# Optimization experiments

Measured on AMD Instinct MI355X. Metric: run time of the kernel, lower is better.

The kernel has to match this reference:

```python
import jax, jax.numpy as jnp
import numpy as np

E, N, D, H = 600000, 100000, 128, 128
LN_EPS = 1e-5


def setup_inputs() -> dict:
    key = jax.random.key(0)
    ks = jax.random.split(key, 10)
    inp = {
        "efeat": jax.random.normal(ks[0], (E, D), dtype=jnp.float32),
        "nfeat": jax.random.normal(ks[1], (N, D), dtype=jnp.float32),
        "src_idx": jax.random.randint(ks[2], (E,), 0, N, dtype=jnp.int64) if jax.config.jax_enable_x64 else jax.random.randint(ks[2], (E,), 0, N, dtype=jnp.int32),
        "dst_idx": jax.random.randint(ks[3], (E,), 0, N, dtype=jnp.int32),
        # MLP params: Linear(3D -> H) + SiLU, Linear(H -> D), LayerNorm(D)
        "W1": jax.random.normal(ks[4], (3 * D, H), dtype=jnp.float32) / np.sqrt(3 * D),
        "b1": jnp.zeros((H,), dtype=jnp.float32),
        "W2": jax.random.normal(ks[5], (H, D), dtype=jnp.float32) / np.sqrt(H),
        "b2": jnp.zeros((D,), dtype=jnp.float32),
        "ln_scale": jnp.ones((D,), dtype=jnp.float32),
        "ln_bias": jnp.zeros((D,), dtype=jnp.float32),
    }
    return inp


def _layernorm(x, scale, bias):
    mu = jnp.mean(x, axis=-1, keepdims=True)
    var = jnp.mean(jnp.square(x - mu), axis=-1, keepdims=True)
    return (x - mu) * jax.lax.rsqrt(var + LN_EPS) * scale + bias


def reference(efeat, nfeat, src_idx, dst_idx, W1, b1, W2, b2, ln_scale, ln_bias):
    # Gather per-edge source/destination node features (irregular access).
    src = nfeat[src_idx]              # [E, D]
    dst = nfeat[dst_idx]              # [E, D]
    # TMLP: equivalent to concat([efeat, src, dst]) @ W1; expressed as split GEMMs
    # so no [E, 3D] concat buffer is materialized.
    Wf, Ws, Wd = W1[:D], W1[D:2 * D], W1[2 * D:]
    h = efeat @ Wf + src @ Ws + dst @ Wd + b1   # [E, H]
    h = jax.nn.silu(h)
    y = h @ W2 + b2                              # [E, D]
    y = _layernorm(y, ln_scale, ln_bias)
    efeat_new = y + efeat                        # residual add
    return (efeat_new, nfeat)
```

## Files before the change

### kernel.cpp

```cpp
#include <hip/hip_runtime.h>
#include <stdint.h>

#define E_N 600000
#define N_N 100000

typedef short short8   __attribute__((ext_vector_type(8)));
typedef short short8a  __attribute__((ext_vector_type(8), may_alias));
typedef float floatx4  __attribute__((ext_vector_type(4)));
typedef float floatx2  __attribute__((ext_vector_type(2)));
typedef float floatx4a __attribute__((ext_vector_type(4), may_alias));
typedef float floatx8a __attribute__((ext_vector_type(8), may_alias));
typedef unsigned int uintx2  __attribute__((ext_vector_type(2)));
typedef unsigned int uintx2a __attribute__((ext_vector_type(2), may_alias));
typedef unsigned int uintx4  __attribute__((ext_vector_type(4)));
typedef unsigned int uintx4a __attribute__((ext_vector_type(4), may_alias));
typedef __bf16 bf16x4 __attribute__((ext_vector_type(4)));
typedef __bf16 bf16x8 __attribute__((ext_vector_type(8)));

static __device__ __forceinline__ unsigned short f2bf(float f){
  unsigned u = __builtin_bit_cast(unsigned, f);
  unsigned rnd = 0x7fffu + ((u >> 16) & 1u);
  return (unsigned short)((u + rnd) >> 16);
}
static __device__ __forceinline__ unsigned pk2(float a, float b){
  floatx2 f; f[0] = a; f[1] = b;
  typedef __bf16 bf16x2 __attribute__((ext_vector_type(2)));
  return __builtin_bit_cast(unsigned, __builtin_convertvector(f, bf16x2));
}

__global__ void prep_weights(const float* __restrict__ W1, const float* __restrict__ W2,
                             unsigned short* __restrict__ wall){
  int i = blockIdx.x * 256 + threadIdx.x;
  if (i < 384 * 128){
    int c = i / 384, k = i - c * 384;
    int win = k >> 6, kp = k & 63;
    wall[win * 8192 + (c * 32 + ((kp >> 1) ^ ((c & 7) << 2))) * 2 + (kp & 1)]
      = f2bf(W1[k * 128 + c]);
  } else {
    int j = i - 384 * 128;
    int c = j >> 7, k = j & 127;
    int win = 6 + (k >> 6), kp = k & 63;
    wall[win * 8192 + (c * 32 + ((kp >> 1) ^ ((c & 7) << 2))) * 2 + (kp & 1)]
      = f2bf(W2[k * 128 + c]);
  }
}

__global__ void prep_nfeat(const float* __restrict__ nf,
                           unsigned* __restrict__ nfbu,
                           float* __restrict__ out2){
  const int total = N_N * 128 / 4;
  int stride = gridDim.x * blockDim.x;
  for (int i = blockIdx.x * blockDim.x + threadIdx.x; i < total; i += stride){
    float4 v = reinterpret_cast<const float4*>(nf)[i];
    reinterpret_cast<float4*>(out2)[i] = v;
    nfbu[2 * i]     = pk2(v.x, v.y);
    nfbu[2 * i + 1] = pk2(v.z, v.w);
  }
}

static __device__ __forceinline__ void glds16(void* lds, const void* g){
  __builtin_amdgcn_global_load_lds((const __attribute__((address_space(1))) unsigned int*)g,
                                   (__attribute__((address_space(3))) unsigned int*)lds,
                                   16, 0, 0);
}

__global__ __launch_bounds__(256, 3) void fused_edge(
    const float* __restrict__ efeat,
    const int* __restrict__ src_idx, const int* __restrict__ dst_idx,
    const unsigned short* __restrict__ nfb,
    const unsigned short* __restrict__ wall,
    const float* __restrict__ b1, const float* __restrict__ b2,
    const float* __restrict__ lns, const float* __restrict__ lnb,
    float* __restrict__ out)
{
  __shared__ __align__(16) unsigned char smem[51200];
  unsigned int* wbuf  = (unsigned int*)smem;
  float*        cmisc = (float*)(smem + 49152);

  const int tid  = threadIdx.x;
  const int w    = tid >> 6;
  const int lane = tid & 63;
  const int r    = lane & 15;
  const int g    = lane >> 4;
  const int sw8  = (r & 7) << 2;

  unsigned int* tile = (unsigned int*)(smem + 32768 + w * 4096);

  auto stageW = [&](int b, int win){
    const unsigned char* src = (const unsigned char*)wall + win * 16384;
    #pragma unroll
    for (int rnd = 0; rnd < 4; ++rnd){
      int off = rnd * 4096 + tid * 16;
      glds16(smem + b * 16384 + off, src + off);
    }
  };

  stageW(0, 0);
  cmisc[tid]       = tid < 128 ? b1[tid]  : b2[tid - 128];
  cmisc[tid + 256] = tid < 128 ? lns[tid] : lnb[tid - 128];

  const int eb = blockIdx.x * 64 + w * 16;
  const int e0 = eb + r;
  int si = src_idx[e0];
  int di = dst_idx[e0];
  si = si < 0 ? 0 : (si >= N_N ? N_N - 1 : si);
  di = di < 0 ? 0 : (di >= N_N ? N_N - 1 : di);

  auto loadX_f32 = [&](const float* p) -> short8 {
    floatx8a f = *reinterpret_cast<const floatx8a*>(p);
    return __builtin_bit_cast(short8, __builtin_convertvector(f, bf16x8));
  };

  short8 xf[12];
  #pragma unroll
  for (int kf = 0; kf < 4; ++kf)
    xf[kf] = loadX_f32(efeat + (size_t)e0 * 128 + kf * 32 + 8 * g);
  #pragma unroll
  for (int kf = 0; kf < 4; ++kf)
    xf[4 + kf] = *reinterpret_cast<const short8a*>(nfb + (size_t)si * 128 + kf * 32 + 8 * g);
  #pragma unroll
  for (int kf = 0; kf < 4; ++kf)
    xf[8 + kf] = *reinterpret_cast<const short8a*>(nfb + (size_t)di * 128 + kf * 32 + 8 * g);

  __syncthreads();

  auto loadWL = [&](int b, int m, int k2) -> short8 {
    uintx4a v = *reinterpret_cast<const uintx4a*>(
        &wbuf[b * 4096 + (16 * m + r) * 32 + ((k2 * 16 + 4 * g) ^ sw8)]);
    return __builtin_bit_cast(short8, v);
  };

  floatx4 acc1[8];
  #pragma unroll
  for (int mi = 0; mi < 8; ++mi)
    acc1[mi] = (floatx4){0.f, 0.f, 0.f, 0.f};

  #pragma unroll
  for (int t = 0; t < 6; ++t){
    stageW((t + 1) & 1, t + 1);
    const int b = t & 1;
    #pragma unroll
    for (int k2 = 0; k2 < 2; ++k2){
      short8 x = xf[2 * t + k2];
      #pragma unroll
      for (int mi = 0; mi < 8; ++mi){
        short8 wf = loadWL(b, mi, k2);
        acc1[mi] = __builtin_amdgcn_mfma_f32_16x16x32_bf16(wf, x, acc1[mi], 0, 0, 0);
      }
    }
    if (t == 5){
      #pragma unroll
      for (int mi = 0; mi < 8; ++mi){
        floatx4 bb = *reinterpret_cast<const floatx4a*>(&cmisc[16 * mi + 4 * g]);
        floatx4 vv;
        #pragma unroll
        for (int q = 0; q < 4; ++q){
          float xx = acc1[mi][q] + bb[q];
          vv[q] = xx * __builtin_amdgcn_rcpf(1.f + __expf(-xx));
        }
        uintx2 pk = __builtin_bit_cast(uintx2, __builtin_convertvector(vv, bf16x4));
        *reinterpret_cast<uintx2a*>(&tile[r * 64 + ((8 * mi + 2 * g) ^ sw8)]) = pk;
      }
    }
    __syncthreads();
  }

  floatx4 acc2[8];
  #pragma unroll
  for (int mo = 0; mo < 8; ++mo)
    acc2[mo] = (floatx4){0.f, 0.f, 0.f, 0.f};

  #pragma unroll
  for (int t = 6; t < 8; ++t){
    if (t < 7) stageW((t + 1) & 1, t + 1);
    const int b = t & 1;
    #pragma unroll
    for (int k2 = 0; k2 < 2; ++k2){
      const int ks = 2 * (t - 6) + k2;
      uintx4a hv = *reinterpret_cast<const uintx4a*>(&tile[r * 64 + ((ks * 16 + 4 * g) ^ sw8)]);
      short8 hb = __builtin_bit_cast(short8, hv);
      #pragma unroll
      for (int mo = 0; mo < 8; ++mo){
        short8 wf = loadWL(b, mo, k2);
        acc2[mo] = __builtin_amdgcn_mfma_f32_16x16x32_bf16(wf, hb, acc2[mo], 0, 0, 0);
      }
    }
    if (t < 7) __syncthreads();
  }

  #pragma unroll
  for (int kf = 0; kf < 4; ++kf)
    *reinterpret_cast<uintx4a*>(&tile[r * 64 + ((16 * kf + 4 * g) ^ sw8)]) =
        __builtin_bit_cast(uintx4, xf[kf]);

  float s1 = 0.f, s2 = 0.f;
  #pragma unroll
  for (int mo = 0; mo < 8; ++mo){
    floatx4 bb = *reinterpret_cast<const floatx4a*>(&cmisc[128 + 16 * mo + 4 * g]);
    #pragma unroll
    for (int q = 0; q < 4; ++q){
      float v = acc2[mo][q] + bb[q];
      s1 += v; s2 += v * v;
    }
  }
  s1 += __shfl_xor(s1, 16); s2 += __shfl_xor(s2, 16);
  s1 += __shfl_xor(s1, 32); s2 += __shfl_xor(s2, 32);

  float mu   = s1 * (1.f / 128.f);
  float var  = s2 * (1.f / 128.f) - mu * mu;
  var = var > 0.f ? var : 0.f;
  float rstd = __builtin_amdgcn_rsqf(var + 1e-5f);

  float* op = out + (size_t)e0 * 128;
  #pragma unroll
  for (int mo = 0; mo < 8; ++mo){
    int c = 16 * mo + 4 * g;
    floatx4 bb = *reinterpret_cast<const floatx4a*>(&cmisc[128 + c]);
    floatx4 ls = *reinterpret_cast<const floatx4a*>(&cmisc[256 + c]);
    floatx4 lb = *reinterpret_cast<const floatx4a*>(&cmisc[384 + c]);
    uintx2a rv = *reinterpret_cast<const uintx2a*>(&tile[r * 64 + ((8 * mo + 2 * g) ^ sw8)]);
    floatx4 e4;
    e4[0] = __builtin_bit_cast(float, rv[0] << 16);
    e4[1] = __builtin_bit_cast(float, rv[0] & 0xffff0000u);
    e4[2] = __builtin_bit_cast(float, rv[1] << 16);
    e4[3] = __builtin_bit_cast(float, rv[1] & 0xffff0000u);
    floatx4 o4;
    #pragma unroll
    for (int q = 0; q < 4; ++q)
      o4[q] = (acc2[mo][q] + bb[q] - mu) * rstd * ls[q] + lb[q] + e4[q];
    *reinterpret_cast<floatx4a*>(op + c) = o4;
  }
}

extern "C" void kernel_launch(void* const* d_in, const int* in_sizes, int n_in,
                              void* d_out, int out_size, void* d_ws, size_t ws_size,
                              hipStream_t stream){
  const float* efeat = (const float*)d_in[0];
  const float* nfeat = (const float*)d_in[1];
  const int*   srci  = (const int*)d_in[2];
  const int*   dsti  = (const int*)d_in[3];
  const float* W1    = (const float*)d_in[4];
  const float* b1    = (const float*)d_in[5];
  const float* W2    = (const float*)d_in[6];
  const float* b2    = (const float*)d_in[7];
  const float* lns   = (const float*)d_in[8];
  const float* lnb   = (const float*)d_in[9];
  float* out = (float*)d_out;

  char* ws = (char*)d_ws;
  unsigned short* wall = (unsigned short*)ws;
  unsigned short* nfb  = (unsigned short*)(ws + 131072);

  prep_weights<<<(384 * 128 + 128 * 128) / 256, 256, 0, stream>>>(W1, W2, wall);
  prep_nfeat<<<2048, 256, 0, stream>>>(nfeat, (unsigned*)nfb, out + (size_t)E_N * 128);

  int blocks = E_N / 64;
  fused_edge<<<blocks, 256, 0, stream>>>(efeat, srci, dsti, nfb, wall,
                                         b1, b2, lns, lnb, out);
}
```

Measured before the change: 234.2 us.

## Switch fused edge kernel to 32x32x16 MFMA with register-resident hidden activations

```diff
diff --git a/kernel.cpp b/kernel.cpp
--- a/kernel.cpp
+++ b/kernel.cpp
@@ -6,12 +6,12 @@
 
 typedef short short8   __attribute__((ext_vector_type(8)));
 typedef short short8a  __attribute__((ext_vector_type(8), may_alias));
+typedef float floatx2  __attribute__((ext_vector_type(2)));
 typedef float floatx4  __attribute__((ext_vector_type(4)));
-typedef float floatx2  __attribute__((ext_vector_type(2)));
+typedef float floatx16 __attribute__((ext_vector_type(16)));
 typedef float floatx4a __attribute__((ext_vector_type(4), may_alias));
 typedef float floatx8a __attribute__((ext_vector_type(8), may_alias));
 typedef unsigned int uintx2  __attribute__((ext_vector_type(2)));
-typedef unsigned int uintx2a __attribute__((ext_vector_type(2), may_alias));
 typedef unsigned int uintx4  __attribute__((ext_vector_type(4)));
 typedef unsigned int uintx4a __attribute__((ext_vector_type(4), may_alias));
 typedef __bf16 bf16x4 __attribute__((ext_vector_type(4)));
@@ -31,18 +31,17 @@
 __global__ void prep_weights(const float* __restrict__ W1, const float* __restrict__ W2,
                              unsigned short* __restrict__ wall){
   int i = blockIdx.x * 256 + threadIdx.x;
+  int c, k, win; float v;
   if (i < 384 * 128){
-    int c = i / 384, k = i - c * 384;
-    int win = k >> 6, kp = k & 63;
-    wall[win * 8192 + (c * 32 + ((kp >> 1) ^ ((c & 7) << 2))) * 2 + (kp & 1)]
-      = f2bf(W1[k * 128 + c]);
+    c = i / 384; k = i - c * 384; win = k >> 6;
+    v = W1[k * 128 + c];
   } else {
     int j = i - 384 * 128;
-    int c = j >> 7, k = j & 127;
-    int win = 6 + (k >> 6), kp = k & 63;
-    wall[win * 8192 + (c * 32 + ((kp >> 1) ^ ((c & 7) << 2))) * 2 + (kp & 1)]
-      = f2bf(W2[k * 128 + c]);
-  }
+    c = j >> 7; k = j & 127; win = 6 + (k >> 6);
+    v = W2[k * 128 + c];
+  }
+  int kp = k & 63;
+  wall[win * 8192 + (c * 32 + ((kp >> 1) ^ ((c & 7) << 2))) * 2 + (kp & 1)] = f2bf(v);
 }
 
 __global__ void prep_nfeat(const float* __restrict__ nf,
@@ -73,18 +72,16 @@
     const float* __restrict__ lns, const float* __restrict__ lnb,
     float* __restrict__ out)
 {
-  __shared__ __align__(16) unsigned char smem[51200];
+  __shared__ __align__(16) unsigned char smem[34816];
   unsigned int* wbuf  = (unsigned int*)smem;
-  float*        cmisc = (float*)(smem + 49152);
+  float*        cmisc = (float*)(smem + 32768);
 
   const int tid  = threadIdx.x;
   const int w    = tid >> 6;
   const int lane = tid & 63;
-  const int r    = lane & 15;
-  const int g    = lane >> 4;
-  const int sw8  = (r & 7) << 2;
-
-  unsigned int* tile = (unsigned int*)(smem + 32768 + w * 4096);
+  const int rl   = lane & 31;
+  const int hi   = lane >> 5;
+  const int swz  = (rl & 7) << 2;
 
   auto stageW = [&](int b, int win){
     const unsigned char* src = (const unsigned char*)wall + win * 16384;
@@ -99,111 +96,154 @@
   cmisc[tid]       = tid < 128 ? b1[tid]  : b2[tid - 128];
   cmisc[tid + 256] = tid < 128 ? lns[tid] : lnb[tid - 128];
 
-  const int eb = blockIdx.x * 64 + w * 16;
-  const int e0 = eb + r;
-  int si = src_idx[e0];
-  int di = dst_idx[e0];
+  const int e0 = blockIdx.x * 128 + w * 32 + rl;
+  const int ec = e0 < E_N ? e0 : (E_N - 1);
+  int si = src_idx[ec], di = dst_idx[ec];
   si = si < 0 ? 0 : (si >= N_N ? N_N - 1 : si);
   di = di < 0 ? 0 : (di >= N_N ? N_N - 1 : di);
 
-  auto loadX_f32 = [&](const float* p) -> short8 {
-    floatx8a f = *reinterpret_cast<const floatx8a*>(p);
+  auto ldE = [&](int ks8) -> short8 {
+    floatx8a f = *reinterpret_cast<const floatx8a*>(efeat + (size_t)ec * 128 + ks8 * 16 + hi * 8);
     return __builtin_bit_cast(short8, __builtin_convertvector(f, bf16x8));
   };
-
-  short8 xf[12];
-  #pragma unroll
-  for (int kf = 0; kf < 4; ++kf)
-    xf[kf] = loadX_f32(efeat + (size_t)e0 * 128 + kf * 32 + 8 * g);
-  #pragma unroll
-  for (int kf = 0; kf < 4; ++kf)
-    xf[4 + kf] = *reinterpret_cast<const short8a*>(nfb + (size_t)si * 128 + kf * 32 + 8 * g);
-  #pragma unroll
-  for (int kf = 0; kf < 4; ++kf)
-    xf[8 + kf] = *reinterpret_cast<const short8a*>(nfb + (size_t)di * 128 + kf * 32 + 8 * g);
-
-  __syncthreads();
-
-  auto loadWL = [&](int b, int m, int k2) -> short8 {
+  auto ldG = [&](int row, int ks8) -> short8 {
+    return *reinterpret_cast<const short8a*>(nfb + (size_t)row * 128 + ks8 * 16 + hi * 8);
+  };
+
+  short8 xe[8], xc[4], xn[4];
+  #pragma unroll
+  for (int ks8 = 0; ks8 < 8; ++ks8) xe[ks8] = ldE(ks8);
+  #pragma unroll
+  for (int k = 0; k < 4; ++k) xc[k] = ldG(si, k);
+
+  __syncthreads();
+
+  auto loadW = [&](int b, int m, int ks) -> short8 {
     uintx4a v = *reinterpret_cast<const uintx4a*>(
-        &wbuf[b * 4096 + (16 * m + r) * 32 + ((k2 * 16 + 4 * g) ^ sw8)]);
+        &wbuf[b * 4096 + (32 * m + rl) * 32 + ((ks * 8 + hi * 4) ^ swz)]);
     return __builtin_bit_cast(short8, v);
   };
 
-  floatx4 acc1[8];
-  #pragma unroll
-  for (int mi = 0; mi < 8; ++mi)
-    acc1[mi] = (floatx4){0.f, 0.f, 0.f, 0.f};
-
-  #pragma unroll
-  for (int t = 0; t < 6; ++t){
-    stageW((t + 1) & 1, t + 1);
-    const int b = t & 1;
-    #pragma unroll
-    for (int k2 = 0; k2 < 2; ++k2){
-      short8 x = xf[2 * t + k2];
+  floatx16 acc1[4];
+  #pragma unroll
+  for (int mt = 0; mt < 4; ++mt)
+    #pragma unroll
+    for (int q = 0; q < 16; ++q) acc1[mt][q] = 0.f;
+
+  auto g1win = [&](int b, const short8* xs){
+    #pragma unroll
+    for (int ks = 0; ks < 4; ++ks){
       #pragma unroll
-      for (int mi = 0; mi < 8; ++mi){
-        short8 wf = loadWL(b, mi, k2);
-        acc1[mi] = __builtin_amdgcn_mfma_f32_16x16x32_bf16(wf, x, acc1[mi], 0, 0, 0);
+      for (int mt = 0; mt < 4; ++mt){
+        short8 wf = loadW(b, mt, ks);
+        acc1[mt] = __builtin_amdgcn_mfma_f32_32x32x16_bf16(wf, xs[ks], acc1[mt], 0, 0, 0);
       }
     }
-    if (t == 5){
+  };
+
+  stageW(1, 1);
+  #pragma unroll
+  for (int k = 0; k < 4; ++k) xn[k] = ldG(si, 4 + k);
+  g1win(0, xe);
+  __syncthreads();
+
+  stageW(0, 2);
+  g1win(1, xe + 4);
+  __syncthreads();
+
+  stageW(1, 3);
+  g1win(0, xc);
+  #pragma unroll
+  for (int k = 0; k < 4; ++k) xc[k] = ldG(di, k);
+  __syncthreads();
+
+  stageW(0, 4);
+  g1win(1, xn);
+  #pragma unroll
+  for (int k = 0; k < 4; ++k) xn[k] = ldG(di, 4 + k);
+  __syncthreads();
+
+  stageW(1, 5);
+  g1win(0, xc);
+  __syncthreads();
+
+  stageW(0, 6);
+  g1win(1, xn);
+  __syncthreads();
+
+  short8 hfr[8];
+  #pragma unroll
+  for (int mt = 0; mt < 4; ++mt){
+    floatx4 sv[4];
+    #pragma unroll
+    for (int p = 0; p < 4; ++p){
+      floatx4 bb = *reinterpret_cast<const floatx4a*>(&cmisc[32 * mt + 8 * p + 4 * hi]);
       #pragma unroll
-      for (int mi = 0; mi < 8; ++mi){
-        floatx4 bb = *reinterpret_cast<const floatx4a*>(&cmisc[16 * mi + 4 * g]);
-        floatx4 vv;
-        #pragma unroll
-        for (int q = 0; q < 4; ++q){
-          float xx = acc1[mi][q] + bb[q];
-          vv[q] = xx * __builtin_amdgcn_rcpf(1.f + __expf(-xx));
-        }
-        uintx2 pk = __builtin_bit_cast(uintx2, __builtin_convertvector(vv, bf16x4));
-        *reinterpret_cast<uintx2a*>(&tile[r * 64 + ((8 * mi + 2 * g) ^ sw8)]) = pk;
+      for (int i = 0; i < 4; ++i){
+        float xx = acc1[mt][4 * p + i] + bb[i];
+        sv[p][i] = xx * __builtin_amdgcn_rcpf(1.f + __expf(-xx));
       }
     }
-    __syncthreads();
-  }
-
-  floatx4 acc2[8];
-  #pragma unroll
-  for (int mo = 0; mo < 8; ++mo)
-    acc2[mo] = (floatx4){0.f, 0.f, 0.f, 0.f};
-
-  #pragma unroll
-  for (int t = 6; t < 8; ++t){
-    if (t < 7) stageW((t + 1) & 1, t + 1);
-    const int b = t & 1;
-    #pragma unroll
-    for (int k2 = 0; k2 < 2; ++k2){
-      const int ks = 2 * (t - 6) + k2;
-      uintx4a hv = *reinterpret_cast<const uintx4a*>(&tile[r * 64 + ((ks * 16 + 4 * g) ^ sw8)]);
-      short8 hb = __builtin_bit_cast(short8, hv);
+    #pragma unroll
+    for (int k1 = 0; k1 < 2; ++k1){
+      uintx2 P0 = __builtin_bit_cast(uintx2, __builtin_convertvector(sv[2 * k1],     bf16x4));
+      uintx2 P1 = __builtin_bit_cast(uintx2, __builtin_convertvector(sv[2 * k1 + 1], bf16x4));
+      unsigned sA = hi ? P0[0] : P1[0];
+      unsigned sB = hi ? P0[1] : P1[1];
+      unsigned rA = __shfl_xor(sA, 32);
+      unsigned rB = __shfl_xor(sB, 32);
+      uintx4 u;
+      u[0] = hi ? rA : P0[0];
+      u[1] = hi ? rB : P0[1];
+      u[2] = hi ? P1[0] : rA;
+      u[3] = hi ? P1[1] : rB;
+      hfr[2 * mt + k1] = __builtin_bit_cast(short8, u);
+    }
+  }
+
+  uintx2 rk[8], rr[8];
+  #pragma unroll
+  for (int ks = 0; ks < 8; ++ks){
+    uintx4 u = __builtin_bit_cast(uintx4, xe[ks]);
+    unsigned sA = hi ? u[0] : u[2];
+    unsigned sB = hi ? u[1] : u[3];
+    rr[ks][0] = __shfl_xor(sA, 32);
+    rr[ks][1] = __shfl_xor(sB, 32);
+    rk[ks][0] = hi ? u[2] : u[0];
+    rk[ks][1] = hi ? u[3] : u[1];
+  }
+
+  floatx16 acc2[4];
+  #pragma unroll
+  for (int mo = 0; mo < 4; ++mo)
+    #pragma unroll
+    for (int q = 0; q < 16; ++q) acc2[mo][q] = 0.f;
+
+  stageW(1, 7);
+  #pragma unroll
+  for (int ks = 0; ks < 4; ++ks)
+    #pragma unroll
+    for (int mo = 0; mo < 4; ++mo)
+      acc2[mo] = __builtin_amdgcn_mfma_f32_32x32x16_bf16(loadW(0, mo, ks), hfr[ks], acc2[mo], 0, 0, 0);
+  __syncthreads();
+  #pragma unroll
+  for (int ks = 0; ks < 4; ++ks)
+    #pragma unroll
+    for (int mo = 0; mo < 4; ++mo)
+      acc2[mo] = __builtin_amdgcn_mfma_f32_32x32x16_bf16(loadW(1, mo, ks), hfr[4 + ks], acc2[mo], 0, 0, 0);
+
+  float s1 = 0.f, s2 = 0.f;
+  #pragma unroll
+  for (int mt = 0; mt < 4; ++mt)
+    #pragma unroll
+    for (int p = 0; p < 4; ++p){
+      floatx4 bb = *reinterpret_cast<const floatx4a*>(&cmisc[128 + 32 * mt + 8 * p + 4 * hi]);
       #pragma unroll
-      for (int mo = 0; mo < 8; ++mo){
-        short8 wf = loadWL(b, mo, k2);
-        acc2[mo] = __builtin_amdgcn_mfma_f32_16x16x32_bf16(wf, hb, acc2[mo], 0, 0, 0);
+      for (int i = 0; i < 4; ++i){
+        float v = acc2[mt][4 * p + i] + bb[i];
+        s1 += v; s2 += v * v;
       }
     }
-    if (t < 7) __syncthreads();
-  }
-
-  #pragma unroll
-  for (int kf = 0; kf < 4; ++kf)
-    *reinterpret_cast<uintx4a*>(&tile[r * 64 + ((16 * kf + 4 * g) ^ sw8)]) =
-        __builtin_bit_cast(uintx4, xf[kf]);
-
-  float s1 = 0.f, s2 = 0.f;
-  #pragma unroll
-  for (int mo = 0; mo < 8; ++mo){
-    floatx4 bb = *reinterpret_cast<const floatx4a*>(&cmisc[128 + 16 * mo + 4 * g]);
-    #pragma unroll
-    for (int q = 0; q < 4; ++q){
-      float v = acc2[mo][q] + bb[q];
-      s1 += v; s2 += v * v;
-    }
-  }
-  s1 += __shfl_xor(s1, 16); s2 += __shfl_xor(s2, 16);
   s1 += __shfl_xor(s1, 32); s2 += __shfl_xor(s2, 32);
 
   float mu   = s1 * (1.f / 128.f);
@@ -211,24 +251,27 @@
   var = var > 0.f ? var : 0.f;
   float rstd = __builtin_amdgcn_rsqf(var + 1e-5f);
 
-  float* op = out + (size_t)e0 * 128;
-  #pragma unroll
-  for (int mo = 0; mo < 8; ++mo){
-    int c = 16 * mo + 4 * g;
-    floatx4 bb = *reinterpret_cast<const floatx4a*>(&cmisc[128 + c]);
-    floatx4 ls = *reinterpret_cast<const floatx4a*>(&cmisc[256 + c]);
-    floatx4 lb = *reinterpret_cast<const floatx4a*>(&cmisc[384 + c]);
-    uintx2a rv = *reinterpret_cast<const uintx2a*>(&tile[r * 64 + ((8 * mo + 2 * g) ^ sw8)]);
-    floatx4 e4;
-    e4[0] = __builtin_bit_cast(float, rv[0] << 16);
-    e4[1] = __builtin_bit_cast(float, rv[0] & 0xffff0000u);
-    e4[2] = __builtin_bit_cast(float, rv[1] << 16);
-    e4[3] = __builtin_bit_cast(float, rv[1] & 0xffff0000u);
-    floatx4 o4;
-    #pragma unroll
-    for (int q = 0; q < 4; ++q)
-      o4[q] = (acc2[mo][q] + bb[q] - mu) * rstd * ls[q] + lb[q] + e4[q];
-    *reinterpret_cast<floatx4a*>(op + c) = o4;
+  if (e0 < E_N){
+    float* op = out + (size_t)e0 * 128;
+    #pragma unroll
+    for (int mt = 0; mt < 4; ++mt)
+      #pragma unroll
+      for (int p = 0; p < 4; ++p){
+        int c = 32 * mt + 8 * p + 4 * hi;
+        floatx4 bb = *reinterpret_cast<const floatx4a*>(&cmisc[128 + c]);
+        floatx4 ls = *reinterpret_cast<const floatx4a*>(&cmisc[256 + c]);
+        floatx4 lb = *reinterpret_cast<const floatx4a*>(&cmisc[384 + c]);
+        const int ks = 2 * mt + (p >> 1);
+        uintx2 pk_ = ((p & 1) == hi) ? rk[ks] : rr[ks];
+        floatx4 o4;
+        #pragma unroll
+        for (int i = 0; i < 4; ++i){
+          unsigned dwv = pk_[i >> 1];
+          float ef = __builtin_bit_cast(float, (i & 1) ? (dwv & 0xffff0000u) : (dwv << 16));
+          o4[i] = (acc2[mt][4 * p + i] + bb[i] - mu) * rstd * ls[i] + lb[i] + ef;
+        }
+        *reinterpret_cast<floatx4a*>(op + c) = o4;
+      }
   }
 }
 
@@ -254,7 +297,7 @@
   prep_weights<<<(384 * 128 + 128 * 128) / 256, 256, 0, stream>>>(W1, W2, wall);
   prep_nfeat<<<2048, 256, 0, stream>>>(nfeat, (unsigned*)nfb, out + (size_t)E_N * 128);
 
-  int blocks = E_N / 64;
+  int blocks = (E_N + 127) / 128;
   fused_edge<<<blocks, 256, 0, stream>>>(efeat, srci, dsti, nfb, wall,
                                          b1, b2, lns, lnb, out);
 }
```

Result: no change. 231.1 us (-1.3%).
